# Kernel tuning notes

Hardware: AMD Instinct MI355X
Metric: run time of the kernel (lower is better)

## Reference

```python
import math
import jax, jax.numpy as jnp
import numpy as np

B, A, M, NC = 32, 8400, 32, 80
TOP_K, ALPHA, BETA, EPS = 13, 1.0, 6.0, 1e-9
IMG = 640.0


def _ciou(b1, b2, eps=1e-7):
    # b1, b2 broadcastable [..., 4]; CIoU as in compute_iou (box1=gt, box2=pred)
    b1x1, b1y1, b1x2, b1y2 = b1[..., 0], b1[..., 1], b1[..., 2], b1[..., 3]
    b2x1, b2y1, b2x2, b2y2 = b2[..., 0], b2[..., 1], b2[..., 2], b2[..., 3]
    w1, h1 = b1x2 - b1x1, b1y2 - b1y1 + eps
    w2, h2 = b2x2 - b2x1, b2y2 - b2y1 + eps
    inter = (jnp.minimum(b1x2, b2x2) - jnp.maximum(b1x1, b2x1)).clip(0) * \
            (jnp.minimum(b1y2, b2y2) - jnp.maximum(b1y1, b2y1)).clip(0)
    union = w1 * h1 + w2 * h2 - inter + eps
    iou = inter / union
    cw = jnp.maximum(b1x2, b2x2) - jnp.minimum(b1x1, b2x1)
    ch = jnp.maximum(b1y2, b2y2) - jnp.minimum(b1y1, b2y1)
    c2 = cw ** 2 + ch ** 2 + eps
    rho2 = ((b2x1 + b2x2 - b1x1 - b1x2) ** 2 + (b2y1 + b2y2 - b1y1 - b1y2) ** 2) / 4.0
    v = (4.0 / math.pi ** 2) * (jnp.arctan(w2 / h2) - jnp.arctan(w1 / h1)) ** 2
    alpha = jax.lax.stop_gradient(v / (v - iou + (1.0 + eps)))
    return iou - (rho2 / c2 + v * alpha)


def setup_inputs() -> dict:
    key = jax.random.key(0)
    ks = jax.random.split(key, 8)
    pd_scores = jax.random.uniform(ks[0], (B, A, NC), jnp.float32)
    anc_points = jax.random.uniform(ks[1], (A, 2), jnp.float32) * IMG
    # predicted boxes around anchor points (valid x1<x2, y1<y2)
    off = jax.random.uniform(ks[2], (B, A, 4), jnp.float32) * 80.0 + 2.0
    pd_bboxes = jnp.concatenate([anc_points[None] - off[..., :2],
                                 anc_points[None] + off[..., 2:]], -1)
    # GT boxes: random centers and sizes, clipped to image
    c = jax.random.uniform(ks[3], (B, M, 2), jnp.float32) * IMG
    wh = jax.random.uniform(ks[4], (B, M, 2), jnp.float32) * 180.0 + 20.0
    gt_bboxes = jnp.concatenate([(c - wh / 2).clip(0, IMG), (c + wh / 2).clip(0, IMG)], -1)
    gt_labels = jax.random.randint(ks[5], (B, M, 1), 0, NC, jnp.int64)
    n_valid = jax.random.randint(ks[6], (B,), 1, M + 1)
    mask_gt = (jnp.arange(M)[None, :] < n_valid[:, None]).astype(jnp.float32)[..., None]
    return {"pd_scores": pd_scores, "pd_bboxes": pd_bboxes, "anc_points": anc_points,
            "gt_labels": gt_labels, "gt_bboxes": gt_bboxes, "mask_gt": mask_gt}


def reference(pd_scores, pd_bboxes, anc_points, gt_labels, gt_bboxes, mask_gt):
    b, a, nc = pd_scores.shape
    m = gt_bboxes.shape[1]
    dtype = pd_scores.dtype

    # anchors-inside-GT mask: [B,M,A]
    lt = gt_bboxes[:, :, None, :2]          # [B,M,1,2]
    rb = gt_bboxes[:, :, None, 2:]
    deltas = jnp.concatenate([anc_points[None, None] - lt,
                              rb - anc_points[None, None]], -1)  # [B,M,A,4]
    mask_in_gts = deltas.min(-1) > EPS
    mg = mask_gt[..., 0] > 0                 # [B,M] bool
    gt_mask = mask_in_gts & mg[:, :, None]

    # per-GT class score gather: pd_scores[b, :, gt_labels[b,m]] -> [B,M,A]
    labels = gt_labels[..., 0]               # [B,M]
    idx = jnp.broadcast_to(labels[:, :, None, None], (b, m, a, 1))
    gathered = jnp.take_along_axis(jnp.broadcast_to(pd_scores[:, None], (b, m, a, nc)), idx, axis=3)[..., 0]
    bbox_scores = jnp.where(gt_mask, gathered, 0.0)

    # CIoU overlaps (dense, masked) [B,M,A]
    iou = _ciou(gt_bboxes[:, :, None, :], pd_bboxes[:, None, :, :])
    overlaps = jnp.where(gt_mask, jnp.maximum(iou, 0.0), 0.0)

    align_metric = bbox_scores ** ALPHA * overlaps ** BETA

    # top-k selection with duplicate suppression (faithful to scatter_add loop)
    _, tk_idx = jax.lax.top_k(align_metric, TOP_K)      # [B,M,K]
    tk_mask = jnp.broadcast_to(mg[:, :, None], tk_idx.shape)
    tk_idx = jnp.where(tk_mask, tk_idx, 0)
    bi = jnp.arange(b)[:, None, None]
    mi = jnp.arange(m)[None, :, None]
    counts = jnp.zeros((b, m, a), jnp.int32).at[bi, mi, tk_idx].add(1)
    mask_top_k = jnp.where(counts > 1, 0, counts).astype(dtype)

    mask_pos = mask_top_k * mask_in_gts.astype(dtype) * mg[:, :, None].astype(dtype)
    fg_mask = mask_pos.sum(1)                            # [B,A]

    # resolve anchors assigned to multiple GTs (no-op when none; matches torch branch)
    mask_multi = fg_mask[:, None, :] > 1                 # [B,M,A] (broadcast)
    max_idx = overlaps.argmax(1)                         # [B,A]
    is_max = (jnp.arange(m)[None, :, None] == max_idx[:, None, :]).astype(dtype)
    mask_pos = jnp.where(mask_multi, is_max, mask_pos)
    fg_mask = mask_pos.sum(1)

    target_gt_idx = mask_pos.argmax(1)                   # [B,A]
    target_labels = jnp.maximum(jnp.take_along_axis(labels, target_gt_idx, axis=1), 0)
    target_bboxes = jnp.take_along_axis(
        gt_bboxes, jnp.broadcast_to(target_gt_idx[..., None], (b, a, 4)), axis=1)

    target_scores = jax.nn.one_hot(target_labels, NC, dtype=dtype)
    target_scores = jnp.where((fg_mask > 0)[..., None], target_scores, 0.0)

    am = align_metric * mask_pos
    pos_am = am.max(-1, keepdims=True)                   # [B,M,1]
    pos_ov = (overlaps * mask_pos).max(-1, keepdims=True)
    norm = (am * pos_ov / (pos_am + EPS)).max(1)[..., None]  # [B,A,1]
    target_scores = target_scores * norm

    return target_bboxes, target_scores, fg_mask > 0
```

## Files before the change

### kernel.cpp

```cpp
#include <hip/hip_runtime.h>
#include <math.h>

#define BB 32
#define AA 8400
#define MM 32
#define NCC 80
#define TOPK 13
#define CAP 1024
#define NW (AA / 32 + 1)

typedef float nfloat4 __attribute__((ext_vector_type(4)));

__device__ __forceinline__ void wave_argmax(float& v, int& i) {
    #pragma unroll
    for (int off = 32; off > 0; off >>= 1) {
        float ov = __shfl_xor(v, off, 64);
        int oi = __shfl_xor(i, off, 64);
        if (ov > v || (ov == v && oi < i)) { v = ov; i = oi; }
    }
}

__global__ __launch_bounds__(256) void k12_topk(
        const float* __restrict__ pd_scores, const float* __restrict__ pd_bboxes,
        const float* __restrict__ anc, const int* __restrict__ gt_labels,
        const float* __restrict__ gt_bboxes, const float* __restrict__ mask_gt,
        int* __restrict__ sel_idx, float* __restrict__ sel_ov, float* __restrict__ sel_am,
        float* __restrict__ pos_am, float* __restrict__ pos_ov) {
    __shared__ float lval[CAP];
    __shared__ int   lidx[CAP];
    __shared__ float oval[CAP];
    __shared__ unsigned int bmask[NW];
    __shared__ float lw[4][TOPK];
    __shared__ int   li[4][TOPK];
    __shared__ float lo[4][TOPK];
    __shared__ int   wsum[4];
    __shared__ int   s_p, s_sel;
    const float eps = 1e-7f;
    int bm = blockIdx.x;
    int b = bm >> 5;
    int tid = threadIdx.x;
    int lane = tid & 63;
    int wid = tid >> 6;
    if (tid == 0) pos_am[bm] = 0.f;
    if (tid == 1) pos_ov[bm] = 0.f;
    if (tid == 2) s_p = 0;
    if (tid == 3) s_sel = 0;
    if (tid < 16) sel_idx[bm * 16 + tid] = -1;
    if (!(mask_gt[bm] > 0.f)) return;

    for (int i = tid; i < NW; i += 256) bmask[i] = 0u;
    float4 g = reinterpret_cast<const float4*>(gt_bboxes)[bm];

    const float4* anc4 = reinterpret_cast<const float4*>(anc);
    unsigned long long bits = 0ull;
    int c_t = 0;
    #pragma unroll
    for (int j = 0; j < 17; j++) {
        int e = tid + (j << 8);
        if (e < 4200) {
            float4 an = anc4[e];
            float d0 = fminf(fminf(an.x - g.x, an.y - g.y), fminf(g.z - an.x, g.w - an.y));
            float d1 = fminf(fminf(an.z - g.x, an.w - g.y), fminf(g.z - an.z, g.w - an.w));
            if (d0 > 1e-9f) { bits |= 1ull << (2 * j);     c_t++; }
            if (d1 > 1e-9f) { bits |= 1ull << (2 * j + 1); c_t++; }
        }
    }
    int x = c_t;
    #pragma unroll
    for (int off = 1; off < 64; off <<= 1) {
        int y = __shfl_up(x, off, 64);
        if (lane >= off) x += y;
    }
    if (lane == 63) wsum[wid] = x;
    __syncthreads();
    int base = 0;
    #pragma unroll
    for (int w = 0; w < 4; w++) if (w < wid) base += wsum[w];
    int n_c = min(wsum[0] + wsum[1] + wsum[2] + wsum[3], CAP);
    {
        int o = base + x - c_t;
        unsigned long long mm_ = bits;
        while (mm_) {
            int k = __builtin_ctzll(mm_);
            mm_ &= mm_ - 1ull;
            int i = 2 * tid + 512 * (k >> 1) + (k & 1);
            if (o < CAP) lidx[o] = i;
            o++;
        }
    }
    for (int s = n_c + tid; s < CAP; s += 256) { lval[s] = -1.f; lidx[s] = AA; }
    __syncthreads();

    float w1 = g.z - g.x, h1 = g.w - g.y + eps;
    float atg = atanf(w1 / h1);
    float w1h1 = w1 * h1;
    float sgx = g.x + g.z, sgy = g.y + g.w;
    int lab = gt_labels[bm];
    const float4* pbb = reinterpret_cast<const float4*>(pd_bboxes) + (long)b * AA;
    const float* scp = pd_scores + (long)b * AA * NCC + lab;
    int nit = (n_c + 255) >> 8;
    for (int it = 0; it < nit; it++) {
        int s = (it << 8) + tid;
        bool pos = false;
        if (s < n_c) {
            int i = lidx[s];
            float4 pb = pbb[i];
            float sc = scp[(long)i * NCC];
            float w2 = pb.z - pb.x, h2 = pb.w - pb.y + eps;
            float iw = fmaxf(fminf(g.z, pb.z) - fmaxf(g.x, pb.x), 0.f);
            float ih = fmaxf(fminf(g.w, pb.w) - fmaxf(g.y, pb.y), 0.f);
            float inter = iw * ih;
            float uni = w1h1 + w2 * h2 - inter + eps;
            float iou = inter / uni;
            float cw = fmaxf(g.z, pb.z) - fminf(g.x, pb.x);
            float ch = fmaxf(g.w, pb.w) - fminf(g.y, pb.y);
            float c2 = cw * cw + ch * ch + eps;
            float dx = pb.x + pb.z - sgx, dy = pb.y + pb.w - sgy;
            float rho2 = (dx * dx + dy * dy) * 0.25f;
            float dv = atanf(w2 / h2) - atg;
            float v = 0.4052847345693511f * dv * dv;
            float alpha = v / (v - iou + (1.0f + eps));
            float cv = iou - (rho2 / c2 + v * alpha);
            float ov = fmaxf(cv, 0.f);
            float o2 = ov * ov;
            float val = sc * o2 * o2 * o2;
            pos = val > 0.f;
            lval[s] = pos ? val : -1.f;
            oval[s] = ov;
            if (pos) atomicOr(&bmask[i >> 5], 1u << (i & 31));
        }
        unsigned long long pm = __ballot(pos);
        if (lane == 0) atomicAdd(&s_p, (int)__popcll(pm));
    }
    __syncthreads();
    int p = s_p;

    if (p >= TOPK) {
        int s0 = (wid << 8) + lane;
        float v0 = lval[s0], v1 = lval[s0 + 64], v2 = lval[s0 + 128], v3 = lval[s0 + 192];
        int   i0 = lidx[s0], i1 = lidx[s0 + 64], i2 = lidx[s0 + 128], i3 = lidx[s0 + 192];
        for (int k = 0; k < TOPK; k++) {
            float bv = v0; int bi = i0;
            if (v1 > bv || (v1 == bv && i1 < bi)) { bv = v1; bi = i1; }
            if (v2 > bv || (v2 == bv && i2 < bi)) { bv = v2; bi = i2; }
            if (v3 > bv || (v3 == bv && i3 < bi)) { bv = v3; bi = i3; }
            wave_argmax(bv, bi);
            if (i0 == bi) { v0 = -1.f; lo[wid][k] = oval[s0]; }
            if (i1 == bi) { v1 = -1.f; lo[wid][k] = oval[s0 + 64]; }
            if (i2 == bi) { v2 = -1.f; lo[wid][k] = oval[s0 + 128]; }
            if (i3 == bi) { v3 = -1.f; lo[wid][k] = oval[s0 + 192]; }
            if (lane == 0) { lw[wid][k] = bv; li[wid][k] = bi; }
        }
        __syncthreads();
        if (wid == 0) {
            float mv = -1.f; int mi = AA; float mo = 0.f;
            if (lane < 4 * TOPK) {
                int w = lane / TOPK, k = lane - w * TOPK;
                mv = lw[w][k]; mi = li[w][k]; mo = lo[w][k];
            }
            for (int k = 0; k < TOPK; k++) {
                float bv = mv; int bi = mi;
                wave_argmax(bv, bi);
                if (mi == bi && mv > -1.f) {
                    sel_idx[bm * 16 + k] = bi;
                    sel_am[bm * 16 + k] = bv;
                    sel_ov[bm * 16 + k] = mo;
                    mv = -1.f;
                }
            }
        }
    } else {
        for (int s = tid; s < n_c; s += 256)
            if (lval[s] > 0.f) {
                int slot = atomicAdd(&s_sel, 1);
                sel_idx[bm * 16 + slot] = lidx[s];
                sel_ov[bm * 16 + slot] = oval[s];
                sel_am[bm * 16 + slot] = lval[s];
            }
        if (wid == 0) {
            int need = TOPK - p;
            for (int base_i = 0; need > 0 && base_i < AA; base_i += 64) {
                int i = base_i + lane;
                bool cand = (i < AA) && !((bmask[i >> 5] >> (i & 31)) & 1u);
                unsigned long long wm = __ballot(cand);
                int take = min(need, (int)__popcll(wm));
                if (cand && (int)__popcll(wm & ((1ull << lane) - 1ull)) < take) {
                    float2 an = reinterpret_cast<const float2*>(anc)[i];
                    float dmin = fminf(fminf(an.x - g.x, an.y - g.y), fminf(g.z - an.x, g.w - an.y));
                    if (dmin > 1e-9f) {
                        float4 pb = pbb[i];
                        float w2 = pb.z - pb.x, h2 = pb.w - pb.y + eps;
                        float iw = fmaxf(fminf(g.z, pb.z) - fmaxf(g.x, pb.x), 0.f);
                        float ih = fmaxf(fminf(g.w, pb.w) - fmaxf(g.y, pb.y), 0.f);
                        float inter = iw * ih;
                        float uni = w1h1 + w2 * h2 - inter + eps;
                        float iou = inter / uni;
                        float cw = fmaxf(g.z, pb.z) - fminf(g.x, pb.x);
                        float ch = fmaxf(g.w, pb.w) - fminf(g.y, pb.y);
                        float c2 = cw * cw + ch * ch + eps;
                        float dx = pb.x + pb.z - sgx, dy = pb.y + pb.w - sgy;
                        float rho2 = (dx * dx + dy * dy) * 0.25f;
                        float dv = atanf(w2 / h2) - atg;
                        float v = 0.4052847345693511f * dv * dv;
                        float alpha = v / (v - iou + (1.0f + eps));
                        float ov = fmaxf(iou - (rho2 / c2 + v * alpha), 0.f);
                        int slot = atomicAdd(&s_sel, 1);
                        sel_idx[bm * 16 + slot] = i;
                        sel_ov[bm * 16 + slot] = ov;
                        sel_am[bm * 16 + slot] = 0.f;
                    }
                }
                need -= take;
            }
        }
    }
}

__global__ __launch_bounds__(256) void k3_resolve(
        const float* __restrict__ pd_scores, const float* __restrict__ pd_bboxes,
        const float* __restrict__ anc, const int* __restrict__ gt_labels,
        const float* __restrict__ gt_bboxes, const float* __restrict__ mask_gt,
        const int* __restrict__ sel_idx, const float* __restrict__ sel_ov,
        const float* __restrict__ sel_am,
        float* __restrict__ pos_am, float* __restrict__ pos_ov,
        float* __restrict__ out_bbox, float* __restrict__ out_fg,
        int2* __restrict__ meta) {
    __shared__ float sg[MM][8];
    __shared__ int slab[MM];
    __shared__ int smg[MM];
    __shared__ unsigned int selcol[256];
    __shared__ float sov[256];
    __shared__ float sam[256];
    const float eps = 1e-7f;
    int b = blockIdx.y;
    int tid = threadIdx.x;
    if (tid < MM) {
        int gm = b * MM + tid;
        float4 g = reinterpret_cast<const float4*>(gt_bboxes)[gm];
        float w1 = g.z - g.x, h1 = g.w - g.y + eps;
        sg[tid][0] = g.x; sg[tid][1] = g.y; sg[tid][2] = g.z; sg[tid][3] = g.w;
        sg[tid][4] = w1 * h1;
        sg[tid][5] = atanf(w1 / h1);
        sg[tid][6] = g.x + g.z;
        sg[tid][7] = g.y + g.w;
        int lb = gt_labels[gm]; if (lb < 0) lb = 0;
        slab[tid] = lb;
        smg[tid] = mask_gt[gm] > 0.f ? 1 : 0;
    }
    selcol[tid] = 0u;
    __syncthreads();
    int a0 = blockIdx.x * 256;
    const int* sl = sel_idx + b * MM * 16;
    #pragma unroll
    for (int t = tid; t < MM * 16; t += 256) {
        int e = sl[t];
        if (e >= a0 && e < a0 + 256) {
            atomicOr(&selcol[e - a0], 1u << (t >> 4));
            sov[e - a0] = sel_ov[b * MM * 16 + t];
            sam[e - a0] = sel_am[b * MM * 16 + t];
        }
    }
    __syncthreads();
    int a = a0 + tid;
    if (a >= AA) return;
    int g = b * AA + a;
    unsigned int sel = selcol[tid];
    int fg = __popc(sel);

    int tg = 0; bool fgo = false; float ovt = 0.f; float amv = 0.f;
    if (fg == 1) {
        tg = __ffs(sel) - 1;
        ovt = sov[tid];
        amv = sam[tid];
        fgo = true;
    } else if (fg > 1) {
        float ax = anc[a * 2], ay = anc[a * 2 + 1];
        float4 pb = reinterpret_cast<const float4*>(pd_bboxes)[g];
        float w2 = pb.z - pb.x, h2 = pb.w - pb.y + eps;
        float atp = atanf(w2 / h2);
        float w2h2 = w2 * h2;
        float spx = pb.x + pb.z, spy = pb.y + pb.w;
        float bestov = -1.f; int bestm = 0;
        for (int mm = 0; mm < MM; mm++) {
            float gx1 = sg[mm][0], gy1 = sg[mm][1], gx2 = sg[mm][2], gy2 = sg[mm][3];
            float dmin = fminf(fminf(ax - gx1, ay - gy1), fminf(gx2 - ax, gy2 - ay));
            float ov = 0.f;
            if ((dmin > 1e-9f) && smg[mm]) {
                float iw = fmaxf(fminf(gx2, pb.z) - fmaxf(gx1, pb.x), 0.f);
                float ih = fmaxf(fminf(gy2, pb.w) - fmaxf(gy1, pb.y), 0.f);
                float inter = iw * ih;
                float uni = sg[mm][4] + w2h2 - inter + eps;
                float iou = inter / uni;
                float cw = fmaxf(gx2, pb.z) - fminf(gx1, pb.x);
                float ch = fmaxf(gy2, pb.w) - fminf(gy1, pb.y);
                float c2 = cw * cw + ch * ch + eps;
                float dx = spx - sg[mm][6], dy = spy - sg[mm][7];
                float rho2 = (dx * dx + dy * dy) * 0.25f;
                float dv = atp - sg[mm][5];
                float v = 0.4052847345693511f * dv * dv;
                float alpha = v / (v - iou + (1.0f + eps));
                ov = fmaxf(iou - (rho2 / c2 + v * alpha), 0.f);
            }
            if (ov > bestov) { bestov = ov; bestm = mm; }
        }
        tg = bestm; ovt = bestov;
        float sc = pd_scores[(long)g * NCC + slab[tg]];
        float o2 = ovt * ovt;
        amv = sc * o2 * o2 * o2;
        fgo = true;
    }

    nfloat4 gb = {sg[tg][0], sg[tg][1], sg[tg][2], sg[tg][3]};
    __builtin_nontemporal_store(gb, reinterpret_cast<nfloat4*>(out_bbox) + g);
    out_fg[g] = fgo ? 1.f : 0.f;
    if (fgo) {
        atomicMax((int*)&pos_am[b * MM + tg], __float_as_int(amv));
        atomicMax((int*)&pos_ov[b * MM + tg], __float_as_int(ovt));
    }
    meta[g] = make_int2(__float_as_int(amv), tg | (slab[tg] << 8) | ((fgo ? 1 : 0) << 16));
}

__global__ __launch_bounds__(256) void k4_scores(
        const int2* __restrict__ meta,
        const float* __restrict__ pos_am, const float* __restrict__ pos_ov,
        float* __restrict__ out_scores) {
    int g = blockIdx.x * 256 + threadIdx.x;
    const int NQ = NCC / 4;
    if (g >= BB * AA * NQ) return;
    int ba = g / NQ;
    int c0 = (g % NQ) * 4;
    nfloat4 o = {0.f, 0.f, 0.f, 0.f};
    int2 mt = meta[ba];
    int p = mt.y;
    if (p & (1 << 16)) {
        int tg = p & 31, lab = (p >> 8) & 127;
        int b = ba / AA;
        int bm = b * MM + tg;
        float nv = (__int_as_float(mt.x) * pos_ov[bm]) / (pos_am[bm] + 1e-9f);
        int d = lab - c0;
        if (d == 0) o.x = nv; else if (d == 1) o.y = nv;
        else if (d == 2) o.z = nv; else if (d == 3) o.w = nv;
    }
    __builtin_nontemporal_store(o, reinterpret_cast<nfloat4*>(out_scores) + g);
}

extern "C" void kernel_launch(void* const* d_in, const int* in_sizes, int n_in,
                              void* d_out, int out_size, void* d_ws, size_t ws_size,
                              hipStream_t stream) {
    const float* pd_scores = (const float*)d_in[0];
    const float* pd_bboxes = (const float*)d_in[1];
    const float* anc       = (const float*)d_in[2];
    const int*   gt_labels = (const int*)d_in[3];
    const float* gt_bboxes = (const float*)d_in[4];
    const float* mask_gt   = (const float*)d_in[5];

    const long nBA = (long)BB * AA;

    char* ws = (char*)d_ws;
    int*   sel_idx = (int*)ws;                  ws += (long)BB * MM * 16 * 4;
    float* sel_ov  = (float*)ws;                ws += (long)BB * MM * 16 * 4;
    float* sel_am  = (float*)ws;                ws += (long)BB * MM * 16 * 4;
    float* pos_am  = (float*)ws;                ws += BB * MM * 4;
    float* pos_ov  = (float*)ws;                ws += BB * MM * 4;
    int2*  meta    = (int2*)ws;                 ws += nBA * 8;

    float* out_bbox   = (float*)d_out;
    float* out_scores = out_bbox + nBA * 4;
    float* out_fg     = out_scores + nBA * NCC;

    k12_topk<<<BB * MM, 256, 0, stream>>>(pd_scores, pd_bboxes, anc, gt_labels,
                                          gt_bboxes, mask_gt, sel_idx, sel_ov, sel_am,
                                          pos_am, pos_ov);
    dim3 g3((AA + 255) / 256, BB);
    k3_resolve<<<g3, 256, 0, stream>>>(pd_scores, pd_bboxes, anc, gt_labels,
                                       gt_bboxes, mask_gt, sel_idx, sel_ov, sel_am,
                                       pos_am, pos_ov, out_bbox, out_fg, meta);
    long nS4 = nBA * (NCC / 4);
    k4_scores<<<(int)((nS4 + 255) / 256), 256, 0, stream>>>(meta, pos_am, pos_ov, out_scores);
}
```

Baseline: 193.8 us.

## Batch candidate gathers, remap block order, and cap occupancy in topk kernel

The candidate CIoU loop is restructured so each thread issues all four gathers of boxes and scores up front, then computes. This exposes memory-level parallelism instead of serialising load latency per iteration. The block index is remapped so consecutive blocks touch different batches, which changes L2 and channel locality. The launch bounds now request 4 waves per SIMD, which may constrain register allocation. The per-wave count is now reduced with shuffles instead of a ballot per iteration, and slots beyond CAP are assumed unnecessary.

```diff
diff --git a/kernel.cpp b/kernel.cpp
--- a/kernel.cpp
+++ b/kernel.cpp
@@ -20,7 +20,7 @@
     }
 }
 
-__global__ __launch_bounds__(256) void k12_topk(
+__global__ __launch_bounds__(256, 4) void k12_topk(
         const float* __restrict__ pd_scores, const float* __restrict__ pd_bboxes,
         const float* __restrict__ anc, const int* __restrict__ gt_labels,
         const float* __restrict__ gt_bboxes, const float* __restrict__ mask_gt,
@@ -36,8 +36,11 @@
     __shared__ int   wsum[4];
     __shared__ int   s_p, s_sel;
     const float eps = 1e-7f;
-    int bm = blockIdx.x;
-    int b = bm >> 5;
+    int bx = blockIdx.x;
+    int jj = bx >> 3;
+    int b  = (bx & 7) * 4 + (jj >> 5);
+    int m  = jj & 31;
+    int bm = b * MM + m;
     int tid = threadIdx.x;
     int lane = tid & 63;
     int wid = tid >> 6;
@@ -98,39 +101,52 @@
     int lab = gt_labels[bm];
     const float4* pbb = reinterpret_cast<const float4*>(pd_bboxes) + (long)b * AA;
     const float* scp = pd_scores + (long)b * AA * NCC + lab;
-    int nit = (n_c + 255) >> 8;
-    for (int it = 0; it < nit; it++) {
-        int s = (it << 8) + tid;
-        bool pos = false;
-        if (s < n_c) {
-            int i = lidx[s];
-            float4 pb = pbb[i];
-            float sc = scp[(long)i * NCC];
-            float w2 = pb.z - pb.x, h2 = pb.w - pb.y + eps;
-            float iw = fmaxf(fminf(g.z, pb.z) - fmaxf(g.x, pb.x), 0.f);
-            float ih = fmaxf(fminf(g.w, pb.w) - fmaxf(g.y, pb.y), 0.f);
-            float inter = iw * ih;
-            float uni = w1h1 + w2 * h2 - inter + eps;
-            float iou = inter / uni;
-            float cw = fmaxf(g.z, pb.z) - fminf(g.x, pb.x);
-            float ch = fmaxf(g.w, pb.w) - fminf(g.y, pb.y);
-            float c2 = cw * cw + ch * ch + eps;
-            float dx = pb.x + pb.z - sgx, dy = pb.y + pb.w - sgy;
-            float rho2 = (dx * dx + dy * dy) * 0.25f;
-            float dv = atanf(w2 / h2) - atg;
-            float v = 0.4052847345693511f * dv * dv;
-            float alpha = v / (v - iou + (1.0f + eps));
-            float cv = iou - (rho2 / c2 + v * alpha);
-            float ov = fmaxf(cv, 0.f);
-            float o2 = ov * ov;
-            float val = sc * o2 * o2 * o2;
-            pos = val > 0.f;
-            lval[s] = pos ? val : -1.f;
-            oval[s] = ov;
-            if (pos) atomicOr(&bmask[i >> 5], 1u << (i & 31));
-        }
-        unsigned long long pm = __ballot(pos);
-        if (lane == 0) atomicAdd(&s_p, (int)__popcll(pm));
+    {
+        int    ci0, ci1, ci2, ci3;
+        float4 pb0, pb1, pb2, pb3;
+        float  sc0, sc1, sc2, sc3;
+        ci0 = (tid < n_c)       ? lidx[tid]       : -1;
+        ci1 = (tid + 256 < n_c) ? lidx[tid + 256] : -1;
+        ci2 = (tid + 512 < n_c) ? lidx[tid + 512] : -1;
+        ci3 = (tid + 768 < n_c) ? lidx[tid + 768] : -1;
+        if (ci0 >= 0) { pb0 = pbb[ci0]; sc0 = scp[(long)ci0 * NCC]; }
+        if (ci1 >= 0) { pb1 = pbb[ci1]; sc1 = scp[(long)ci1 * NCC]; }
+        if (ci2 >= 0) { pb2 = pbb[ci2]; sc2 = scp[(long)ci2 * NCC]; }
+        if (ci3 >= 0) { pb3 = pbb[ci3]; sc3 = scp[(long)ci3 * NCC]; }
+        int pcnt = 0;
+        #define CIOU_SLOT(CI, PB, SC, S)                                              \
+            if (CI >= 0) {                                                            \
+                float w2 = PB.z - PB.x, h2 = PB.w - PB.y + eps;                       \
+                float iw = fmaxf(fminf(g.z, PB.z) - fmaxf(g.x, PB.x), 0.f);           \
+                float ih = fmaxf(fminf(g.w, PB.w) - fmaxf(g.y, PB.y), 0.f);           \
+                float inter = iw * ih;                                                \
+                float uni = w1h1 + w2 * h2 - inter + eps;                             \
+                float iou = inter / uni;                                              \
+                float cw = fmaxf(g.z, PB.z) - fminf(g.x, PB.x);                       \
+                float ch = fmaxf(g.w, PB.w) - fminf(g.y, PB.y);                       \
+                float c2 = cw * cw + ch * ch + eps;                                   \
+                float dx = PB.x + PB.z - sgx, dy = PB.y + PB.w - sgy;                 \
+                float rho2 = (dx * dx + dy * dy) * 0.25f;                             \
+                float dv = atanf(w2 / h2) - atg;                                      \
+                float v = 0.4052847345693511f * dv * dv;                              \
+                float alpha = v / (v - iou + (1.0f + eps));                           \
+                float cv = iou - (rho2 / c2 + v * alpha);                             \
+                float ov = fmaxf(cv, 0.f);                                            \
+                float o2 = ov * ov;                                                   \
+                float val = SC * o2 * o2 * o2;                   \
+                bool pos = val > 0.f;                                                 \
+                lval[S] = pos ? val : -1.f;                                           \
+                oval[S] = ov;                                                         \
+                if (pos) { atomicOr(&bmask[CI >> 5], 1u << (CI & 31)); pcnt++; }      \
+            }
+        CIOU_SLOT(ci0, pb0, sc0, tid)
+        CIOU_SLOT(ci1, pb1, sc1, tid + 256)
+        CIOU_SLOT(ci2, pb2, sc2, tid + 512)
+        CIOU_SLOT(ci3, pb3, sc3, tid + 768)
+        #undef CIOU_SLOT
+        #pragma unroll
+        for (int off = 32; off > 0; off >>= 1) pcnt += __shfl_xor(pcnt, off, 64);
+        if (lane == 0) atomicAdd(&s_p, pcnt);
     }
     __syncthreads();
     int p = s_p;
```

Measured after the change: 194.9 us. Within noise of the previous version (+0.6%).
